# Performance work log

Measured on AMD Instinct MI355X. Metric: run time of the kernel, lower is better.

## Reference

```python
import jax, jax.numpy as jnp
import numpy as np

B, S, H, NH = 4, 1024, 1024, 16
HD = H // NH
SCALE = float(np.sqrt(HD))


def setup_inputs() -> dict:
    key = jax.random.key(0)
    ks = jax.random.split(key, 20)
    d = {}
    for i, name in enumerate(["query", "key", "query_side", "key_side", "value"]):
        d[name] = jax.random.normal(ks[i], (B, S, H), dtype=jnp.float32)
    d["mask"] = jax.random.bernoulli(ks[5], 0.5, (B, 1, S, S))
    # linear params (torch nn.Linear convention: y = x @ W.T + b)
    pnames = [("Wq", "bq"), ("Wk", "bk"), ("Wqs", "bqs"), ("Wks", "bks"), ("Wv", "bv"), ("Wo", "bo")]
    lim = 1.0 / np.sqrt(H)
    for j, (wn, bn) in enumerate(pnames):
        d[wn] = jax.random.uniform(ks[6 + 2 * j], (H, H), jnp.float32, -lim, lim)
        d[bn] = jax.random.uniform(ks[7 + 2 * j], (H,), jnp.float32, -lim, lim)
    return d


def _heads(x, W, b):
    # [B,S,H] -> [B,NH,S,HD]
    y = x @ W.T + b
    return y.reshape(x.shape[0], -1, NH, HD).transpose(0, 2, 1, 3)


def reference(query, key, query_side, key_side, value, mask,
              Wq, bq, Wk, bk, Wqs, bqs, Wks, bks, Wv, bv, Wo, bo):
    Q = _heads(query, Wq, bq)
    K = _heads(key, Wk, bk)
    Qs = _heads(query_side, Wqs, bqs)
    Ks = _heads(key_side, Wks, bks)
    V = _heads(value, Wv, bv)

    energy = jnp.einsum("bhqd,bhkd->bhqk", Q, K) / SCALE
    energy_side = jnp.einsum("bhqd,bhkd->bhqk", Qs, Ks) / SCALE
    # masked_fill(mask,0) on energy + masked_fill(mask==0,0) on energy_side
    # == where(mask, energy_side, energy)
    energy = jnp.where(mask, energy_side, energy)

    attention = jax.nn.softmax(energy, axis=-1)
    x = jnp.einsum("bhqk,bhkd->bhqd", attention, V)  # dropout is eval-mode identity
    x = x.transpose(0, 2, 1, 3).reshape(query.shape[0], -1, H)
    x = x @ Wo.T + bo
    return (x, attention)
```

## Files before the change

### kernel.cpp

```cpp
#include <hip/hip_runtime.h>
#include <hip/hip_bf16.h>
#include <stdint.h>

typedef uint16_t u16;
typedef __attribute__((ext_vector_type(8))) short bf16x8;
typedef __attribute__((ext_vector_type(4))) float f32x4;

#define DEVI static __device__ __forceinline__
#define GLOAD_LDS(gptr, lptr) \
  __builtin_amdgcn_global_load_lds((const __attribute__((address_space(1))) void*)(gptr), \
                                   (__attribute__((address_space(3))) void*)(lptr), 16, 0, 0)

constexpr int Bc = 4, Sc = 1024, Hc = 1024, NHc = 16, HDc = 64;
constexpr int Mrows = Bc * Sc;

DEVI u16 f2bf(float f) {
  uint32_t u = __builtin_bit_cast(uint32_t, f);
  u += 0x7FFFu + ((u >> 16) & 1u);
  return (u16)(u >> 16);
}
DEVI float bf2f(u16 x) { return __builtin_bit_cast(float, (uint32_t)x << 16); }

DEVI f32x4 mfma16(bf16x8 a, bf16x8 b, f32x4 c) {
  return __builtin_amdgcn_mfma_f32_16x16x32_bf16(a, b, c, 0, 0, 0);
}

struct CV { const float* in[6]; u16* out[6]; };

__global__ __launch_bounds__(256) void cvtN_kernel(CV a, int n8) {
  int z = blockIdx.z;
  int i = blockIdx.x * 256 + threadIdx.x;
  if (i >= n8) return;
  const f32x4* p = (const f32x4*)(a.in[z] + (size_t)i * 8);
  f32x4 x = p[0], y = p[1];
  union { bf16x8 v; u16 s[8]; } r;
#pragma unroll
  for (int j = 0; j < 4; ++j) { r.s[j] = f2bf(x[j]); r.s[4 + j] = f2bf(y[j]); }
  *(bf16x8*)(a.out[z] + (size_t)i * 8) = r.v;
}

__global__ __launch_bounds__(256) void maskpack_kernel(const int* __restrict__ mask,
                                                       uint32_t* __restrict__ out) {
  int i = blockIdx.x * 256 + threadIdx.x;
  const int4* p = (const int4*)(mask + (size_t)i * 32);
  uint32_t r = 0;
#pragma unroll
  for (int j = 0; j < 8; ++j) {
    int4 v = p[j];
    uint32_t nib = (v.x ? 1u : 0u) | (v.y ? 2u : 0u) | (v.z ? 4u : 0u) | (v.w ? 8u : 0u);
    r |= nib << (j * 4);
  }
  out[i] = r;
}

struct P5 { const u16* A[5]; const u16* W[5]; const float* b[5]; u16* o[5]; };

__global__ __launch_bounds__(256) void proj5_kernel(P5 args) {
  constexpr int K = 1024, BK = 32;
  __shared__ u16 As[128 * BK];
  __shared__ u16 Bs[128 * BK];
  const int z = blockIdx.z;
  const u16* __restrict__ A = args.A[z];
  const u16* __restrict__ Bw = args.W[z];
  const float* __restrict__ bias = args.b[z];
  u16* __restrict__ Cout = args.o[z];
  const int t = threadIdx.x;
  const int w = t >> 6, l = t & 63;
  const int lr = l & 15, lh = l >> 4;
  const int m0 = blockIdx.y * 128, n0 = blockIdx.x * 128;
  const int wr = w >> 1, wc = w & 1;
  f32x4 acc[4][4] = {};

  const int row_s = t >> 2, k8 = (t & 3) << 3;
  const u16* ga = A + (size_t)(m0 + row_s) * K + k8;
  const u16* gb = Bw + (size_t)(n0 + row_s) * K + k8;

  for (int kt = 0; kt < K; kt += BK) {
    GLOAD_LDS(ga + kt, As + t * 8);
    GLOAD_LDS(ga + (size_t)64 * K + kt, As + 2048 + t * 8);
    GLOAD_LDS(gb + kt, Bs + t * 8);
    GLOAD_LDS(gb + (size_t)64 * K + kt, Bs + 2048 + t * 8);
    __syncthreads();
    bf16x8 af[4], bfr[4];
#pragma unroll
    for (int mi = 0; mi < 4; ++mi)
      af[mi] = *(const bf16x8*)(As + (wr * 64 + mi * 16 + lr) * BK + lh * 8);
#pragma unroll
    for (int ni = 0; ni < 4; ++ni)
      bfr[ni] = *(const bf16x8*)(Bs + (wc * 64 + ni * 16 + lr) * BK + lh * 8);
#pragma unroll
    for (int mi = 0; mi < 4; ++mi)
#pragma unroll
      for (int ni = 0; ni < 4; ++ni)
        acc[mi][ni] = mfma16(af[mi], bfr[ni], acc[mi][ni]);
    __syncthreads();
  }

#pragma unroll
  for (int mi = 0; mi < 4; ++mi) {
#pragma unroll
    for (int ni = 0; ni < 4; ++ni) {
      int col = n0 + wc * 64 + ni * 16 + lr;
      float bc = bias[col];
      int hcol = col >> 6, dcol = col & 63;
      int rbase = m0 + wr * 64 + mi * 16 + lh * 4;
      int bb = rbase >> 10, sb = rbase & 1023;
      if (z == 4) {
        ushort4 pk;
        pk.x = f2bf(acc[mi][ni][0] + bc);
        pk.y = f2bf(acc[mi][ni][1] + bc);
        pk.z = f2bf(acc[mi][ni][2] + bc);
        pk.w = f2bf(acc[mi][ni][3] + bc);
        *(ushort4*)&Cout[((size_t)(bb * NHc + hcol) * HDc + dcol) * Sc + sb] = pk;
      } else {
#pragma unroll
        for (int r = 0; r < 4; ++r)
          Cout[((size_t)(bb * NHc + hcol) * Sc + (sb + r)) * HDc + dcol] =
              f2bf(acc[mi][ni][r] + bc);
      }
    }
  }
}

__global__ __launch_bounds__(256) void gemmo_kernel(const u16* __restrict__ A,
                                                    const u16* __restrict__ Bw,
                                                    const float* __restrict__ bias,
                                                    float* __restrict__ Cout) {
  constexpr int K = 1024, N = 1024, BK = 32;
  __shared__ u16 As[128 * BK];
  __shared__ u16 Bs[128 * BK];
  const int t = threadIdx.x;
  const int w = t >> 6, l = t & 63;
  const int lr = l & 15, lh = l >> 4;
  const int m0 = blockIdx.y * 128, n0 = blockIdx.x * 128;
  const int wr = w >> 1, wc = w & 1;
  f32x4 acc[4][4] = {};

  const int row_s = t >> 2, k8 = (t & 3) << 3;
  const u16* ga = A + (size_t)(m0 + row_s) * K + k8;
  const u16* gb = Bw + (size_t)(n0 + row_s) * K + k8;

  for (int kt = 0; kt < K; kt += BK) {
    GLOAD_LDS(ga + kt, As + t * 8);
    GLOAD_LDS(ga + (size_t)64 * K + kt, As + 2048 + t * 8);
    GLOAD_LDS(gb + kt, Bs + t * 8);
    GLOAD_LDS(gb + (size_t)64 * K + kt, Bs + 2048 + t * 8);
    __syncthreads();
    bf16x8 af[4], bfr[4];
#pragma unroll
    for (int mi = 0; mi < 4; ++mi)
      af[mi] = *(const bf16x8*)(As + (wr * 64 + mi * 16 + lr) * BK + lh * 8);
#pragma unroll
    for (int ni = 0; ni < 4; ++ni)
      bfr[ni] = *(const bf16x8*)(Bs + (wc * 64 + ni * 16 + lr) * BK + lh * 8);
#pragma unroll
    for (int mi = 0; mi < 4; ++mi)
#pragma unroll
      for (int ni = 0; ni < 4; ++ni)
        acc[mi][ni] = mfma16(af[mi], bfr[ni], acc[mi][ni]);
    __syncthreads();
  }

#pragma unroll
  for (int mi = 0; mi < 4; ++mi) {
#pragma unroll
    for (int ni = 0; ni < 4; ++ni) {
      int col = n0 + wc * 64 + ni * 16 + lr;
      float bc = bias[col];
#pragma unroll
      for (int r = 0; r < 4; ++r) {
        int rowg = m0 + wr * 64 + mi * 16 + lh * 4 + r;
        Cout[(size_t)rowg * N + col] = acc[mi][ni][r] + bc;
      }
    }
  }
}

__global__ __launch_bounds__(256, 3) void attn_kernel(const u16* __restrict__ Qh,
                                                      const u16* __restrict__ Kh,
                                                      const u16* __restrict__ Qsh,
                                                      const u16* __restrict__ Ksh,
                                                      const u16* __restrict__ Vth,
                                                      const uint32_t* __restrict__ mbits,
                                                      float* __restrict__ Pout,
                                                      u16* __restrict__ ctx) {
  __shared__ __align__(16) u16 E[16 * 1024];
  const int t = threadIdx.x, w = t >> 6, l = t & 63;
  const int lr = l & 15, lh = l >> 4;
  int lid = blockIdx.y * 64 + blockIdx.x;
  int xcd = lid & 7, j = lid >> 3;
  int bh = xcd * 8 + (j >> 6);
  int q0 = (j & 63) << 4;
  const int b = bh >> 4, h = bh & 15;
  const size_t hoff = (size_t)bh * Sc * HDc;

  const u16* Qp = Qh + hoff + (size_t)(q0 + lr) * HDc + lh * 8;
  const u16* Qsp = Qsh + hoff + (size_t)(q0 + lr) * HDc + lh * 8;
  bf16x8 qf0 = *(const bf16x8*)Qp, qf1 = *(const bf16x8*)(Qp + 32);
  bf16x8 sf0 = *(const bf16x8*)Qsp, sf1 = *(const bf16x8*)(Qsp + 32);

  const u16* Kbase = Kh + hoff + (size_t)((w << 8) + lr) * HDc + lh * 8;
  const u16* Ksbase = Ksh + hoff + (size_t)((w << 8) + lr) * HDc + lh * 8;
  const uint32_t* mrow_l = mbits + ((size_t)b * Sc + q0 + lr) * 32 + w * 8;

#pragma unroll
  for (int kt = 0; kt < 16; ++kt) {
    const u16* Kp = Kbase + kt * (16 * HDc);
    const u16* Ksp = Ksbase + kt * (16 * HDc);
    f32x4 e = {}, es = {};
    e = mfma16(*(const bf16x8*)Kp, qf0, e);
    e = mfma16(*(const bf16x8*)(Kp + 32), qf1, e);
    es = mfma16(*(const bf16x8*)Ksp, sf0, es);
    es = mfma16(*(const bf16x8*)(Ksp + 32), sf1, es);
    uint32_t md = mrow_l[kt >> 1];
    int sh = ((kt & 1) << 4) + (lh << 2);
    ushort4 wb;
    wb.x = f2bf(((md >> (sh + 0)) & 1u ? es[0] : e[0]) * 0.125f);
    wb.y = f2bf(((md >> (sh + 1)) & 1u ? es[1] : e[1]) * 0.125f);
    wb.z = f2bf(((md >> (sh + 2)) & 1u ? es[2] : e[2]) * 0.125f);
    wb.w = f2bf(((md >> (sh + 3)) & 1u ? es[3] : e[3]) * 0.125f);
    int kb = (w << 8) + (kt << 4) + (lh << 2);
    int kg = kb >> 3;
    *(ushort4*)&E[(lr << 10) + (((kg ^ (lr & 7)) << 3) | (kb & 7))] = wb;
  }
  __syncthreads();

  float* Pbase = Pout + ((size_t)bh * Sc + q0) * Sc;
#pragma unroll
  for (int rr = 0; rr < 4; ++rr) {
    int row = (w << 2) + rr;
    int sw = row & 7;
    float v[4][4];
#pragma unroll
    for (int jj = 0; jj < 4; ++jj) {
      int k = jj * 256 + (l << 2);
      ushort4 raw = *(const ushort4*)&E[(row << 10) + ((((k >> 3) ^ sw) << 3) | (k & 7))];
      v[jj][0] = bf2f(raw.x); v[jj][1] = bf2f(raw.y);
      v[jj][2] = bf2f(raw.z); v[jj][3] = bf2f(raw.w);
    }
    float m = -1e30f;
#pragma unroll
    for (int jj = 0; jj < 4; ++jj)
      m = fmaxf(m, fmaxf(fmaxf(v[jj][0], v[jj][1]), fmaxf(v[jj][2], v[jj][3])));
#pragma unroll
    for (int off = 32; off; off >>= 1) m = fmaxf(m, __shfl_xor(m, off));
    float s = 0.f;
#pragma unroll
    for (int jj = 0; jj < 4; ++jj)
#pragma unroll
      for (int i = 0; i < 4; ++i) { float tt = __expf(v[jj][i] - m); v[jj][i] = tt; s += tt; }
#pragma unroll
    for (int off = 32; off; off >>= 1) s += __shfl_xor(s, off);
    float inv = 1.f / s;
#pragma unroll
    for (int jj = 0; jj < 4; ++jj) {
      int k = jj * 256 + (l << 2);
      f32x4 pv = { v[jj][0] * inv, v[jj][1] * inv, v[jj][2] * inv, v[jj][3] * inv };
      __builtin_nontemporal_store(pv, (f32x4*)(Pbase + (size_t)row * Sc + k));
      ushort4 wb;
      wb.x = f2bf(pv[0]); wb.y = f2bf(pv[1]); wb.z = f2bf(pv[2]); wb.w = f2bf(pv[3]);
      *(ushort4*)&E[(row << 10) + ((((k >> 3) ^ sw) << 3) | (k & 7))] = wb;
    }
  }
  __syncthreads();

  const u16* Vb = Vth + ((size_t)bh * HDc + (w << 4) + lr) * Sc + lh * 8;
  const int swp = lr & 7;
  f32x4 acc0 = {}, acc1 = {};
#pragma unroll
  for (int k0 = 0; k0 < 1024; k0 += 64) {
    int ka = k0 + (lh << 3);
    bf16x8 a0 = *(const bf16x8*)&E[(lr << 10) + (((ka >> 3) ^ swp) << 3)];
    bf16x8 b0 = *(const bf16x8*)(Vb + k0);
    acc0 = mfma16(a0, b0, acc0);
    int kb = ka + 32;
    bf16x8 a1 = *(const bf16x8*)&E[(lr << 10) + (((kb >> 3) ^ swp) << 3)];
    bf16x8 b1 = *(const bf16x8*)(Vb + k0 + 32);
    acc1 = mfma16(a1, b1, acc1);
  }
  f32x4 acc = acc0 + acc1;
#pragma unroll
  for (int r = 0; r < 4; ++r) {
    int row = q0 + (lh << 2) + r;
    ctx[((size_t)b * Sc + row) * Hc + (h << 6) + (w << 4) + lr] = f2bf(acc[r]);
  }
}

extern "C" void kernel_launch(void* const* d_in, const int* in_sizes, int n_in,
                              void* d_out, int out_size, void* d_ws, size_t ws_size,
                              hipStream_t stream) {
  const float* fin[5] = { (const float*)d_in[0], (const float*)d_in[1], (const float*)d_in[2],
                          (const float*)d_in[3], (const float*)d_in[4] };
  const int* mask = (const int*)d_in[5];
  const float* W[6] = { (const float*)d_in[6], (const float*)d_in[8], (const float*)d_in[10],
                        (const float*)d_in[12], (const float*)d_in[14], (const float*)d_in[16] };
  const float* bias[6] = { (const float*)d_in[7], (const float*)d_in[9], (const float*)d_in[11],
                           (const float*)d_in[13], (const float*)d_in[15], (const float*)d_in[17] };

  float* out_x = (float*)d_out;
  float* out_attn = out_x + (size_t)Bc * Sc * Hc;

  const size_t NE = (size_t)Bc * Sc * Hc;
  const size_t NW = (size_t)Hc * Hc;
  u16* p = (u16*)d_ws;
  u16* xin[5]; for (int i = 0; i < 5; ++i) { xin[i] = p; p += NE; }
  u16* wbf[6]; for (int i = 0; i < 6; ++i) { wbf[i] = p; p += NW; }
  u16* Qh  = p; p += NE;
  u16* Kh  = p; p += NE;
  u16* Qsh = p; p += NE;
  u16* Ksh = p; p += NE;
  u16* Vth = p; p += NE;
  u16* ctx = p; p += NE;
  uint32_t* mbits = (uint32_t*)xin[0];

  {
    CV a{};
    for (int i = 0; i < 5; ++i) { a.in[i] = fin[i]; a.out[i] = xin[i]; }
    cvtN_kernel<<<dim3((int)(NE / 8 / 256), 1, 5), 256, 0, stream>>>(a, (int)(NE / 8));
  }
  {
    CV a{};
    for (int i = 0; i < 6; ++i) { a.in[i] = W[i]; a.out[i] = wbf[i]; }
    cvtN_kernel<<<dim3((int)(NW / 8 / 256), 1, 6), 256, 0, stream>>>(a, (int)(NW / 8));
  }

  P5 args;
  u16* projout[5] = { Qh, Kh, Qsh, Ksh, Vth };
  for (int i = 0; i < 5; ++i) { args.A[i] = xin[i]; args.W[i] = wbf[i]; args.b[i] = bias[i]; args.o[i] = projout[i]; }
  proj5_kernel<<<dim3(Hc / 128, Mrows / 128, 5), 256, 0, stream>>>(args);

  maskpack_kernel<<<(int)((size_t)Bc * Sc * Sc / 32 / 256), 256, 0, stream>>>(mask, mbits);

  attn_kernel<<<dim3(Sc / 16, Bc * NHc), 256, 0, stream>>>(Qh, Kh, Qsh, Ksh, Vth, mbits, out_attn, ctx);

  gemmo_kernel<<<dim3(Hc / 128, Mrows / 128), 256, 0, stream>>>(ctx, wbf[5], bias[5], out_x);
}
```

Baseline: 330.0 us.

## Keep attention scores in registers and prefetch K/V tiles in software

Each wave now keeps its masked, scaled score tile as fp32 in registers instead of rounding to bf16 in LDS and reading it back. The row max and sum are reduced across the four waves through small shared arrays, which removes one LDS round trip and the separate softmax pass. K, K_side and V fragments are loaded a few iterations ahead through register ring buffers, and the mask words are loaded once up front, to hide global latency. The cost is much higher register use (64 floats of scores plus the prefetch buffers), which may cut occupancy below the three blocks per CU that the launch bounds target.

After: 343.8 us. 1.04x slower.

```diff
diff --git a/kernel.cpp b/kernel.cpp
--- a/kernel.cpp
+++ b/kernel.cpp
@@ -185,6 +185,8 @@
                                                       float* __restrict__ Pout,
                                                       u16* __restrict__ ctx) {
   __shared__ __align__(16) u16 E[16 * 1024];
+  __shared__ float redM[4][16];
+  __shared__ float redS[4][16];
   const int t = threadIdx.x, w = t >> 6, l = t & 63;
   const int lr = l & 15, lh = l >> 4;
   int lid = blockIdx.y * 64 + blockIdx.x;
@@ -199,85 +201,101 @@
   bf16x8 qf0 = *(const bf16x8*)Qp, qf1 = *(const bf16x8*)(Qp + 32);
   bf16x8 sf0 = *(const bf16x8*)Qsp, sf1 = *(const bf16x8*)(Qsp + 32);
 
+  uint32_t mwreg[8];
+  {
+    const uint32_t* mrow_l = mbits + ((size_t)b * Sc + q0 + lr) * 32 + w * 8;
+    *(uint4*)&mwreg[0] = *(const uint4*)mrow_l;
+    *(uint4*)&mwreg[4] = *(const uint4*)(mrow_l + 4);
+  }
+
   const u16* Kbase = Kh + hoff + (size_t)((w << 8) + lr) * HDc + lh * 8;
   const u16* Ksbase = Ksh + hoff + (size_t)((w << 8) + lr) * HDc + lh * 8;
-  const uint32_t* mrow_l = mbits + ((size_t)b * Sc + q0 + lr) * 32 + w * 8;
-
+
+  bf16x8 ka[3], kb[3], sa[3], sb[3];
+#define LOADK(slot, it) do { \
+    const u16* Kp_ = Kbase + (it) * (16 * HDc); \
+    const u16* Sp_ = Ksbase + (it) * (16 * HDc); \
+    ka[slot] = *(const bf16x8*)Kp_;  kb[slot] = *(const bf16x8*)(Kp_ + 32); \
+    sa[slot] = *(const bf16x8*)Sp_;  sb[slot] = *(const bf16x8*)(Sp_ + 32); } while (0)
+
+  LOADK(0, 0); LOADK(1, 1); LOADK(2, 2);
+
+  f32x4 p[16];
 #pragma unroll
   for (int kt = 0; kt < 16; ++kt) {
-    const u16* Kp = Kbase + kt * (16 * HDc);
-    const u16* Ksp = Ksbase + kt * (16 * HDc);
+    const int s = kt % 3;
     f32x4 e = {}, es = {};
-    e = mfma16(*(const bf16x8*)Kp, qf0, e);
-    e = mfma16(*(const bf16x8*)(Kp + 32), qf1, e);
-    es = mfma16(*(const bf16x8*)Ksp, sf0, es);
-    es = mfma16(*(const bf16x8*)(Ksp + 32), sf1, es);
-    uint32_t md = mrow_l[kt >> 1];
+    e = mfma16(ka[s], qf0, e);
+    e = mfma16(kb[s], qf1, e);
+    es = mfma16(sa[s], sf0, es);
+    es = mfma16(sb[s], sf1, es);
+    if (kt + 3 < 16) LOADK(s, kt + 3);
+    uint32_t md = mwreg[kt >> 1];
     int sh = ((kt & 1) << 4) + (lh << 2);
+    f32x4 r;
+    r[0] = ((md >> (sh + 0)) & 1u ? es[0] : e[0]) * 0.125f;
+    r[1] = ((md >> (sh + 1)) & 1u ? es[1] : e[1]) * 0.125f;
+    r[2] = ((md >> (sh + 2)) & 1u ? es[2] : e[2]) * 0.125f;
+    r[3] = ((md >> (sh + 3)) & 1u ? es[3] : e[3]) * 0.125f;
+    p[kt] = r;
+  }
+#undef LOADK
+
+  float m = -1e30f;
+#pragma unroll
+  for (int kt = 0; kt < 16; ++kt)
+    m = fmaxf(m, fmaxf(fmaxf(p[kt][0], p[kt][1]), fmaxf(p[kt][2], p[kt][3])));
+  m = fmaxf(m, __shfl_xor(m, 16));
+  m = fmaxf(m, __shfl_xor(m, 32));
+  if (lh == 0) redM[w][lr] = m;
+  __syncthreads();
+  m = fmaxf(fmaxf(redM[0][lr], redM[1][lr]), fmaxf(redM[2][lr], redM[3][lr]));
+
+  float sum = 0.f;
+#pragma unroll
+  for (int kt = 0; kt < 16; ++kt) {
+#pragma unroll
+    for (int i = 0; i < 4; ++i) { float tt = __expf(p[kt][i] - m); p[kt][i] = tt; sum += tt; }
+  }
+  sum += __shfl_xor(sum, 16);
+  sum += __shfl_xor(sum, 32);
+  if (lh == 0) redS[w][lr] = sum;
+  __syncthreads();
+  const float inv = 1.f / (redS[0][lr] + redS[1][lr] + redS[2][lr] + redS[3][lr]);
+
+  float* Prow = Pout + ((size_t)bh * Sc + q0 + lr) * Sc + (w << 8) + (lh << 2);
+#pragma unroll
+  for (int kt = 0; kt < 16; ++kt) {
+    f32x4 pv = p[kt] * inv;
+    __builtin_nontemporal_store(pv, (f32x4*)(Prow + (kt << 4)));
     ushort4 wb;
-    wb.x = f2bf(((md >> (sh + 0)) & 1u ? es[0] : e[0]) * 0.125f);
-    wb.y = f2bf(((md >> (sh + 1)) & 1u ? es[1] : e[1]) * 0.125f);
-    wb.z = f2bf(((md >> (sh + 2)) & 1u ? es[2] : e[2]) * 0.125f);
-    wb.w = f2bf(((md >> (sh + 3)) & 1u ? es[3] : e[3]) * 0.125f);
-    int kb = (w << 8) + (kt << 4) + (lh << 2);
-    int kg = kb >> 3;
-    *(ushort4*)&E[(lr << 10) + (((kg ^ (lr & 7)) << 3) | (kb & 7))] = wb;
-  }
+    wb.x = f2bf(pv[0]); wb.y = f2bf(pv[1]); wb.z = f2bf(pv[2]); wb.w = f2bf(pv[3]);
+    int kb16 = (w << 8) + (kt << 4) + (lh << 2);
+    *(ushort4*)&E[(lr << 10) + ((((kb16 >> 3) ^ (lr & 7)) << 3) | (kb16 & 7))] = wb;
+  }
+
+  const u16* Vbp = Vth + ((size_t)bh * HDc + (w << 4) + lr) * Sc + lh * 8;
+  bf16x8 va[2], vb[2];
+#define LOADV(slot, it) do { \
+    va[slot] = *(const bf16x8*)(Vbp + (it) * 64); \
+    vb[slot] = *(const bf16x8*)(Vbp + (it) * 64 + 32); } while (0)
+  LOADV(0, 0); LOADV(1, 1);
+
   __syncthreads();
 
-  float* Pbase = Pout + ((size_t)bh * Sc + q0) * Sc;
-#pragma unroll
-  for (int rr = 0; rr < 4; ++rr) {
-    int row = (w << 2) + rr;
-    int sw = row & 7;
-    float v[4][4];
-#pragma unroll
-    for (int jj = 0; jj < 4; ++jj) {
-      int k = jj * 256 + (l << 2);
-      ushort4 raw = *(const ushort4*)&E[(row << 10) + ((((k >> 3) ^ sw) << 3) | (k & 7))];
-      v[jj][0] = bf2f(raw.x); v[jj][1] = bf2f(raw.y);
-      v[jj][2] = bf2f(raw.z); v[jj][3] = bf2f(raw.w);
-    }
-    float m = -1e30f;
-#pragma unroll
-    for (int jj = 0; jj < 4; ++jj)
-      m = fmaxf(m, fmaxf(fmaxf(v[jj][0], v[jj][1]), fmaxf(v[jj][2], v[jj][3])));
-#pragma unroll
-    for (int off = 32; off; off >>= 1) m = fmaxf(m, __shfl_xor(m, off));
-    float s = 0.f;
-#pragma unroll
-    for (int jj = 0; jj < 4; ++jj)
-#pragma unroll
-      for (int i = 0; i < 4; ++i) { float tt = __expf(v[jj][i] - m); v[jj][i] = tt; s += tt; }
-#pragma unroll
-    for (int off = 32; off; off >>= 1) s += __shfl_xor(s, off);
-    float inv = 1.f / s;
-#pragma unroll
-    for (int jj = 0; jj < 4; ++jj) {
-      int k = jj * 256 + (l << 2);
-      f32x4 pv = { v[jj][0] * inv, v[jj][1] * inv, v[jj][2] * inv, v[jj][3] * inv };
-      __builtin_nontemporal_store(pv, (f32x4*)(Pbase + (size_t)row * Sc + k));
-      ushort4 wb;
-      wb.x = f2bf(pv[0]); wb.y = f2bf(pv[1]); wb.z = f2bf(pv[2]); wb.w = f2bf(pv[3]);
-      *(ushort4*)&E[(row << 10) + ((((k >> 3) ^ sw) << 3) | (k & 7))] = wb;
-    }
-  }
-  __syncthreads();
-
-  const u16* Vb = Vth + ((size_t)bh * HDc + (w << 4) + lr) * Sc + lh * 8;
   const int swp = lr & 7;
   f32x4 acc0 = {}, acc1 = {};
 #pragma unroll
-  for (int k0 = 0; k0 < 1024; k0 += 64) {
-    int ka = k0 + (lh << 3);
-    bf16x8 a0 = *(const bf16x8*)&E[(lr << 10) + (((ka >> 3) ^ swp) << 3)];
-    bf16x8 b0 = *(const bf16x8*)(Vb + k0);
-    acc0 = mfma16(a0, b0, acc0);
-    int kb = ka + 32;
-    bf16x8 a1 = *(const bf16x8*)&E[(lr << 10) + (((kb >> 3) ^ swp) << 3)];
-    bf16x8 b1 = *(const bf16x8*)(Vb + k0 + 32);
-    acc1 = mfma16(a1, b1, acc1);
-  }
+  for (int it = 0; it < 16; ++it) {
+    const int s = it & 1;
+    int ka16 = (it << 6) + (lh << 3);
+    bf16x8 a0 = *(const bf16x8*)&E[(lr << 10) + (((ka16 >> 3) ^ swp) << 3)];
+    bf16x8 a1 = *(const bf16x8*)&E[(lr << 10) + ((((ka16 + 32) >> 3) ^ swp) << 3)];
+    acc0 = mfma16(a0, va[s], acc0);
+    acc1 = mfma16(a1, vb[s], acc1);
+    if (it + 2 < 16) LOADV(s, it + 2);
+  }
+#undef LOADV
   f32x4 acc = acc0 + acc1;
 #pragma unroll
   for (int r = 0; r < 4; ++r) {
```

## Process 32 query rows per attention block and double-buffer K and V loads

Applied to the files above, without the earlier changes.

The attention kernel now covers 32 query rows per block instead of 16, so each K, Ks and V fragment loaded from global memory feeds twice as many MFMAs. K/Ks and V fragments are prefetched two iterations ahead into register slots, and mask words are loaded up front as vectors. LDS grows to 64KB and launch bounds drop to 2 blocks per CU, which lowers occupancy and halves the grid. The probability store also changes from nontemporal to a regular store.

Measured after the change: 290.6 us. 12.0% less time.

```diff
diff --git a/kernel.cpp b/kernel.cpp
--- a/kernel.cpp
+++ b/kernel.cpp
@@ -176,64 +176,100 @@
   }
 }
 
-__global__ __launch_bounds__(256, 3) void attn_kernel(const u16* __restrict__ Qh,
-                                                      const u16* __restrict__ Kh,
-                                                      const u16* __restrict__ Qsh,
-                                                      const u16* __restrict__ Ksh,
-                                                      const u16* __restrict__ Vth,
-                                                      const uint32_t* __restrict__ mbits,
-                                                      float* __restrict__ Pout,
-                                                      u16* __restrict__ ctx) {
-  __shared__ __align__(16) u16 E[16 * 1024];
+__global__ __launch_bounds__(256, 2) void attn5_kernel(const u16* __restrict__ Qh,
+                                                       const u16* __restrict__ Kh,
+                                                       const u16* __restrict__ Qsh,
+                                                       const u16* __restrict__ Ksh,
+                                                       const u16* __restrict__ Vth,
+                                                       const uint32_t* __restrict__ mbits,
+                                                       float* __restrict__ Pout,
+                                                       u16* __restrict__ ctx) {
+  __shared__ __align__(16) u16 E[32 * 1024];
   const int t = threadIdx.x, w = t >> 6, l = t & 63;
   const int lr = l & 15, lh = l >> 4;
-  int lid = blockIdx.y * 64 + blockIdx.x;
+  int lid = blockIdx.y * 32 + blockIdx.x;
   int xcd = lid & 7, j = lid >> 3;
-  int bh = xcd * 8 + (j >> 6);
-  int q0 = (j & 63) << 4;
+  int bh = xcd * 8 + (j >> 5);
+  int q0 = (j & 31) << 5;
   const int b = bh >> 4, h = bh & 15;
   const size_t hoff = (size_t)bh * Sc * HDc;
 
-  const u16* Qp = Qh + hoff + (size_t)(q0 + lr) * HDc + lh * 8;
-  const u16* Qsp = Qsh + hoff + (size_t)(q0 + lr) * HDc + lh * 8;
-  bf16x8 qf0 = *(const bf16x8*)Qp, qf1 = *(const bf16x8*)(Qp + 32);
-  bf16x8 sf0 = *(const bf16x8*)Qsp, sf1 = *(const bf16x8*)(Qsp + 32);
+  const u16* QpA = Qh + hoff + (size_t)(q0 + lr) * HDc + lh * 8;
+  const u16* QspA = Qsh + hoff + (size_t)(q0 + lr) * HDc + lh * 8;
+  bf16x8 qfA0 = *(const bf16x8*)QpA, qfA1 = *(const bf16x8*)(QpA + 32);
+  bf16x8 sfA0 = *(const bf16x8*)QspA, sfA1 = *(const bf16x8*)(QspA + 32);
+  bf16x8 qfB0 = *(const bf16x8*)(QpA + 16 * HDc), qfB1 = *(const bf16x8*)(QpA + 16 * HDc + 32);
+  bf16x8 sfB0 = *(const bf16x8*)(QspA + 16 * HDc), sfB1 = *(const bf16x8*)(QspA + 16 * HDc + 32);
+
+  uint32_t mwA[8], mwB[8];
+  {
+    const uint32_t* mA = mbits + ((size_t)b * Sc + q0 + lr) * 32 + w * 8;
+    *(uint4*)&mwA[0] = *(const uint4*)mA;
+    *(uint4*)&mwA[4] = *(const uint4*)(mA + 4);
+    const uint32_t* mB = mA + 16 * 32;
+    *(uint4*)&mwB[0] = *(const uint4*)mB;
+    *(uint4*)&mwB[4] = *(const uint4*)(mB + 4);
+  }
 
   const u16* Kbase = Kh + hoff + (size_t)((w << 8) + lr) * HDc + lh * 8;
   const u16* Ksbase = Ksh + hoff + (size_t)((w << 8) + lr) * HDc + lh * 8;
-  const uint32_t* mrow_l = mbits + ((size_t)b * Sc + q0 + lr) * 32 + w * 8;
+
+  bf16x8 ka[2], kb[2], sa[2], sb[2];
+#define LOADK(slot, it) do { \
+    const u16* Kp_ = Kbase + (it) * (16 * HDc); \
+    const u16* Sp_ = Ksbase + (it) * (16 * HDc); \
+    ka[slot] = *(const bf16x8*)Kp_;  kb[slot] = *(const bf16x8*)(Kp_ + 32); \
+    sa[slot] = *(const bf16x8*)Sp_;  sb[slot] = *(const bf16x8*)(Sp_ + 32); } while (0)
+
+  LOADK(0, 0); LOADK(1, 1);
 
 #pragma unroll
   for (int kt = 0; kt < 16; ++kt) {
-    const u16* Kp = Kbase + kt * (16 * HDc);
-    const u16* Ksp = Ksbase + kt * (16 * HDc);
-    f32x4 e = {}, es = {};
-    e = mfma16(*(const bf16x8*)Kp, qf0, e);
-    e = mfma16(*(const bf16x8*)(Kp + 32), qf1, e);
-    es = mfma16(*(const bf16x8*)Ksp, sf0, es);
-    es = mfma16(*(const bf16x8*)(Ksp + 32), sf1, es);
-    uint32_t md = mrow_l[kt >> 1];
-    int sh = ((kt & 1) << 4) + (lh << 2);
-    ushort4 wb;
-    wb.x = f2bf(((md >> (sh + 0)) & 1u ? es[0] : e[0]) * 0.125f);
-    wb.y = f2bf(((md >> (sh + 1)) & 1u ? es[1] : e[1]) * 0.125f);
-    wb.z = f2bf(((md >> (sh + 2)) & 1u ? es[2] : e[2]) * 0.125f);
-    wb.w = f2bf(((md >> (sh + 3)) & 1u ? es[3] : e[3]) * 0.125f);
-    int kb = (w << 8) + (kt << 4) + (lh << 2);
-    int kg = kb >> 3;
-    *(ushort4*)&E[(lr << 10) + (((kg ^ (lr & 7)) << 3) | (kb & 7))] = wb;
-  }
+    const int s = kt & 1;
+    f32x4 eA = {}, esA = {}, eB = {}, esB = {};
+    eA = mfma16(ka[s], qfA0, eA);
+    eA = mfma16(kb[s], qfA1, eA);
+    esA = mfma16(sa[s], sfA0, esA);
+    esA = mfma16(sb[s], sfA1, esA);
+    eB = mfma16(ka[s], qfB0, eB);
+    eB = mfma16(kb[s], qfB1, eB);
+    esB = mfma16(sa[s], sfB0, esB);
+    esB = mfma16(sb[s], sfB1, esB);
+    if (kt + 2 < 16) LOADK(s, kt + 2);
+    const int sh = ((kt & 1) << 4) + (lh << 2);
+    const int kb16 = (w << 8) + (kt << 4) + (lh << 2);
+    const int sphys = ((((kb16 >> 3) ^ (lr & 7)) << 3) | (kb16 & 7));
+    {
+      uint32_t md = mwA[kt >> 1];
+      ushort4 wb;
+      wb.x = f2bf(((md >> (sh + 0)) & 1u ? esA[0] : eA[0]) * 0.125f);
+      wb.y = f2bf(((md >> (sh + 1)) & 1u ? esA[1] : eA[1]) * 0.125f);
+      wb.z = f2bf(((md >> (sh + 2)) & 1u ? esA[2] : eA[2]) * 0.125f);
+      wb.w = f2bf(((md >> (sh + 3)) & 1u ? esA[3] : eA[3]) * 0.125f);
+      *(ushort4*)&E[(lr << 10) + sphys] = wb;
+    }
+    {
+      uint32_t md = mwB[kt >> 1];
+      ushort4 wb;
+      wb.x = f2bf(((md >> (sh + 0)) & 1u ? esB[0] : eB[0]) * 0.125f);
+      wb.y = f2bf(((md >> (sh + 1)) & 1u ? esB[1] : eB[1]) * 0.125f);
+      wb.z = f2bf(((md >> (sh + 2)) & 1u ? esB[2] : eB[2]) * 0.125f);
+      wb.w = f2bf(((md >> (sh + 3)) & 1u ? esB[3] : eB[3]) * 0.125f);
+      *(ushort4*)&E[((lr + 16) << 10) + sphys] = wb;
+    }
+  }
+#undef LOADK
   __syncthreads();
 
-  float* Pbase = Pout + ((size_t)bh * Sc + q0) * Sc;
-#pragma unroll
-  for (int rr = 0; rr < 4; ++rr) {
-    int row = (w << 2) + rr;
-    int sw = row & 7;
+  float* Pb = Pout + ((size_t)bh * Sc + q0) * Sc;
+#pragma unroll
+  for (int r8 = 0; r8 < 8; ++r8) {
+    const int row = (w << 3) + r8;
+    const int sw = row & 7;
     float v[4][4];
 #pragma unroll
     for (int jj = 0; jj < 4; ++jj) {
-      int k = jj * 256 + (l << 2);
+      int k = (jj << 8) + (l << 2);
       ushort4 raw = *(const ushort4*)&E[(row << 10) + ((((k >> 3) ^ sw) << 3) | (k & 7))];
       v[jj][0] = bf2f(raw.x); v[jj][1] = bf2f(raw.y);
       v[jj][2] = bf2f(raw.z); v[jj][3] = bf2f(raw.w);
@@ -243,46 +279,62 @@
     for (int jj = 0; jj < 4; ++jj)
       m = fmaxf(m, fmaxf(fmaxf(v[jj][0], v[jj][1]), fmaxf(v[jj][2], v[jj][3])));
 #pragma unroll
-    for (int off = 32; off; off >>= 1) m = fmaxf(m, __shfl_xor(m, off));
-    float s = 0.f;
+    for (int off = 1; off < 64; off <<= 1) m = fmaxf(m, __shfl_xor(m, off));
+    float sum = 0.f;
 #pragma unroll
     for (int jj = 0; jj < 4; ++jj)
 #pragma unroll
-      for (int i = 0; i < 4; ++i) { float tt = __expf(v[jj][i] - m); v[jj][i] = tt; s += tt; }
-#pragma unroll
-    for (int off = 32; off; off >>= 1) s += __shfl_xor(s, off);
-    float inv = 1.f / s;
+      for (int i = 0; i < 4; ++i) { float tt = __expf(v[jj][i] - m); v[jj][i] = tt; sum += tt; }
+#pragma unroll
+    for (int off = 1; off < 64; off <<= 1) sum += __shfl_xor(sum, off);
+    const float inv = 1.f / sum;
 #pragma unroll
     for (int jj = 0; jj < 4; ++jj) {
-      int k = jj * 256 + (l << 2);
+      int k = (jj << 8) + (l << 2);
       f32x4 pv = { v[jj][0] * inv, v[jj][1] * inv, v[jj][2] * inv, v[jj][3] * inv };
-      __builtin_nontemporal_store(pv, (f32x4*)(Pbase + (size_t)row * Sc + k));
+      *(f32x4*)(Pb + (size_t)row * Sc + k) = pv;
       ushort4 wb;
       wb.x = f2bf(pv[0]); wb.y = f2bf(pv[1]); wb.z = f2bf(pv[2]); wb.w = f2bf(pv[3]);
       *(ushort4*)&E[(row << 10) + ((((k >> 3) ^ sw) << 3) | (k & 7))] = wb;
     }
   }
+
+  const u16* Vbp = Vth + ((size_t)bh * HDc + (w << 4) + lr) * Sc + lh * 8;
+  bf16x8 va[2], vb[2];
+#define LOADV(slot, it) do { \
+    va[slot] = *(const bf16x8*)(Vbp + (it) * 64); \
+    vb[slot] = *(const bf16x8*)(Vbp + (it) * 64 + 32); } while (0)
+  LOADV(0, 0); LOADV(1, 1);
+
   __syncthreads();
 
-  const u16* Vb = Vth + ((size_t)bh * HDc + (w << 4) + lr) * Sc + lh * 8;
   const int swp = lr & 7;
-  f32x4 acc0 = {}, acc1 = {};
-#pragma unroll
-  for (int k0 = 0; k0 < 1024; k0 += 64) {
-    int ka = k0 + (lh << 3);
-    bf16x8 a0 = *(const bf16x8*)&E[(lr << 10) + (((ka >> 3) ^ swp) << 3)];
-    bf16x8 b0 = *(const bf16x8*)(Vb + k0);
-    acc0 = mfma16(a0, b0, acc0);
-    int kb = ka + 32;
-    bf16x8 a1 = *(const bf16x8*)&E[(lr << 10) + (((kb >> 3) ^ swp) << 3)];
-    bf16x8 b1 = *(const bf16x8*)(Vb + k0 + 32);
-    acc1 = mfma16(a1, b1, acc1);
-  }
-  f32x4 acc = acc0 + acc1;
+  f32x4 accA0 = {}, accA1 = {}, accB0 = {}, accB1 = {};
+#pragma unroll
+  for (int it = 0; it < 16; ++it) {
+    const int s = it & 1;
+    int ka16 = (it << 6) + (lh << 3);
+    int offL = (((ka16 >> 3) ^ swp) << 3);
+    int offH = ((((ka16 + 32) >> 3) ^ swp) << 3);
+    bf16x8 aA0 = *(const bf16x8*)&E[(lr << 10) + offL];
+    bf16x8 aA1 = *(const bf16x8*)&E[(lr << 10) + offH];
+    bf16x8 aB0 = *(const bf16x8*)&E[((lr + 16) << 10) + offL];
+    bf16x8 aB1 = *(const bf16x8*)&E[((lr + 16) << 10) + offH];
+    accA0 = mfma16(aA0, va[s], accA0);
+    accA1 = mfma16(aA1, vb[s], accA1);
+    accB0 = mfma16(aB0, va[s], accB0);
+    accB1 = mfma16(aB1, vb[s], accB1);
+    if (it + 2 < 16) LOADV(s, it + 2);
+  }
+#undef LOADV
+  f32x4 accA = accA0 + accA1;
+  f32x4 accB = accB0 + accB1;
 #pragma unroll
   for (int r = 0; r < 4; ++r) {
-    int row = q0 + (lh << 2) + r;
-    ctx[((size_t)b * Sc + row) * Hc + (h << 6) + (w << 4) + lr] = f2bf(acc[r]);
+    int rowA = q0 + (lh << 2) + r;
+    ctx[((size_t)b * Sc + rowA) * Hc + (h << 6) + (w << 4) + lr] = f2bf(accA[r]);
+    int rowB = rowA + 16;
+    ctx[((size_t)b * Sc + rowB) * Hc + (h << 6) + (w << 4) + lr] = f2bf(accB[r]);
   }
 }
 
@@ -331,7 +383,7 @@
 
   maskpack_kernel<<<(int)((size_t)Bc * Sc * Sc / 32 / 256), 256, 0, stream>>>(mask, mbits);
 
-  attn_kernel<<<dim3(Sc / 16, Bc * NHc), 256, 0, stream>>>(Qh, Kh, Qsh, Ksh, Vth, mbits, out_attn, ctx);
+  attn5_kernel<<<dim3(Sc / 32, Bc * NHc), 256, 0, stream>>>(Qh, Kh, Qsh, Ksh, Vth, mbits, out_attn, ctx);
 
   gemmo_kernel<<<dim3(Hc / 128, Mrows / 128), 256, 0, stream>>>(ctx, wbf[5], bias[5], out_x);
 }
```
